# Performance work log

Measured on AMD Instinct MI355X. Metric: run time of the kernel, lower is better.

## Reference

```python
import jax, jax.numpy as jnp
import numpy as np
from jax import lax

IMG_W = 1024.0
IMG_H = 1024.0
CONF_THRESH = 0.5
NMS_THRESH = 0.3
MAX_DELTA = 2.0
K_PRE = 300   # pre-NMS candidates per image per level
K_OUT = 10    # keep[:10] per image per level, as in the torch code


def _make_anchors(hw, stride, base, scales=(0.5, 1.0, 1.5), ars=(0.5, 1.0, 2.0)):
    # anchor index a is outermost to match permute(0,1,3,4,2).reshape ordering
    whs = np.array([[base * sc * np.sqrt(ar), base * sc / np.sqrt(ar)]
                    for sc in scales for ar in ars], dtype=np.float32)  # [A,2]
    c = (np.arange(hw, dtype=np.float32) + 0.5) * stride
    cy, cx = np.meshgrid(c, c, indexing='ij')
    cx = cx.reshape(-1)[None, :]  # [1,HW]
    cy = cy.reshape(-1)[None, :]
    w = whs[:, 0:1]
    h = whs[:, 1:2]
    anc = np.stack([cx - 0.5 * w, cy - 0.5 * h, cx + 0.5 * w, cy + 0.5 * h], axis=-1)  # [A,HW,4]
    return jnp.asarray(anc.reshape(-1, 4))


def setup_inputs() -> dict:
    key = jax.random.key(0)
    ks = jax.random.split(key, 8)
    B, A = 16, 9
    hws = [128, 64, 32, 16]
    strides = [8, 16, 32, 64]
    bases = [64, 128, 256, 512]
    inp = {}
    for li in range(4):
        inp[f'cls{li}'] = jax.random.normal(ks[li], (B, A, 1, hws[li], hws[li]), jnp.float32)
        inp[f'box{li}'] = 0.3 * jax.random.normal(ks[li + 4], (B, A, 4, hws[li], hws[li]), jnp.float32)
        inp[f'anc{li}'] = _make_anchors(hws[li], strides[li], bases[li])
    return inp


def decode_boxes(deltas, anchors):
    # deltas: [B,N,4], anchors: [1,N,4] (broadcast). Faithful to apply_deltas_to_anchors.
    w = anchors[..., 2] - anchors[..., 0]
    h = anchors[..., 3] - anchors[..., 1]
    cx = anchors[..., 0] + 0.5 * w
    cy = anchors[..., 1] + 0.5 * h
    d = jnp.clip(deltas, -MAX_DELTA, MAX_DELTA)
    px = cx + d[..., 0] * w
    py = cy + d[..., 1] * h
    pw = w * jnp.exp(d[..., 2])
    ph = h * jnp.exp(d[..., 3])
    x1 = jnp.clip(px - 0.5 * pw, 0.0, IMG_W)
    y1 = jnp.clip(py - 0.5 * ph, 0.0, IMG_H)
    x2 = jnp.clip(px + 0.5 * pw, 0.0, IMG_W)
    y2 = jnp.clip(py + 0.5 * ph, 0.0, IMG_H)
    boxes = jnp.stack([x1, y1, x2, y2], axis=-1)
    bw = x2 - x1
    bh = y2 - y1
    valid = (bw > 1.0) & (bh > 1.0) & (bw < 2000.0) & (bh < 2000.0)
    return boxes, valid


def _pairwise_iou(b):
    # b: [K,4]
    area = (b[:, 2] - b[:, 0]) * (b[:, 3] - b[:, 1])
    x1 = jnp.maximum(b[:, None, 0], b[None, :, 0])
    y1 = jnp.maximum(b[:, None, 1], b[None, :, 1])
    x2 = jnp.minimum(b[:, None, 2], b[None, :, 2])
    y2 = jnp.minimum(b[:, None, 3], b[None, :, 3])
    inter = jnp.clip(x2 - x1, 0.0) * jnp.clip(y2 - y1, 0.0)
    return inter / (area[:, None] + area[None, :] - inter + 1e-9)


def _nms_image(boxes, masked_scores):
    # boxes: [N,4]; masked_scores: [N] (score if conf&valid else -1)
    topv, topi = lax.top_k(masked_scores, K_PRE)   # score-descending, like torchvision nms order
    b = boxes[topi]                                 # [K,4]
    ious = _pairwise_iou(b)
    idxs = jnp.arange(K_PRE)
    keep0 = topv > 0.0  # only candidates above conf thresh (>0.5) survive the mask fill of -1

    def body(i, keep):
        sup = (ious[i] > NMS_THRESH) & (idxs > i)
        return jnp.where(keep[i], keep & ~sup, keep)

    keep = lax.fori_loop(0, K_PRE, body, keep0)
    rank = jnp.cumsum(keep.astype(jnp.int32)) - 1
    sel = keep & (rank < K_OUT)                     # keep[:10]
    idx = jnp.where(sel, rank, K_OUT)               # dump slot K_OUT
    out_b = jnp.zeros((K_OUT + 1, 4), boxes.dtype).at[idx].set(b)[:K_OUT]
    out_s = jnp.zeros((K_OUT + 1,), topv.dtype).at[idx].set(topv)[:K_OUT]
    out_v = jnp.zeros((K_OUT + 1,), bool).at[idx].set(sel)[:K_OUT]
    return out_b, out_s, out_v


def _process_level(cls, box, anc):
    B = cls.shape[0]
    # [B,A,C,H,W] -> [B,A,H,W,C] -> [B,N]; C=1
    scores = jax.nn.sigmoid(jnp.transpose(cls, (0, 1, 3, 4, 2)).reshape(B, -1))
    deltas = jnp.transpose(box, (0, 1, 3, 4, 2)).reshape(B, -1, 4)
    pboxes, valid = decode_boxes(deltas, anc[None])
    masked = jnp.where((scores > CONF_THRESH) & valid, scores, -1.0)
    return jax.vmap(_nms_image)(pboxes, masked)  # ([B,10,4],[B,10],[B,10])


def reference(cls0, cls1, cls2, cls3, box0, box1, box2, box3, anc0, anc1, anc2, anc3):
    levels = [(cls0, box0, anc0), (cls1, box1, anc1), (cls2, box2, anc2), (cls3, box3, anc3)]
    outs = [_process_level(c, b, a) for (c, b, a) in levels]
    boxes = jnp.concatenate([o[0] for o in outs], axis=1)   # [B, 40, 4]
    scores = jnp.concatenate([o[1] for o in outs], axis=1)  # [B, 40]
    valid = jnp.concatenate([o[2] for o in outs], axis=1)   # [B, 40] bool
    out5 = jnp.concatenate([boxes, scores[..., None]], axis=-1)  # [B, 40, 5]
    return out5, valid
```

## Files before the change

### kernel.cpp

```cpp
#include <hip/hip_runtime.h>
#include <stdint.h>

#define NLEV 4
#define BIMG 16
#define NPROB 64
#define NB 1024
#define BUF 2048
#define CPI 97
#define TCH (BIMG * CPI)
#define SKN 6144
#define FK 512
#define SLOTS 8
#define KPRE 300
#define KOUT 10
#define NTHREADS 256
#define CHUNK 2048

__device__ unsigned long long g_cand[TCH * BUF];
__device__ int g_ccount[TCH];

struct Params {
    const float* cls[NLEV];
    const float* box[NLEV];
    const float* anc[NLEV];
};

__device__ __constant__ int c_tbin[4] = {256, 179, 77, 0};
__device__ __constant__ int c_sh[4]   = {14, 12, 10, 8};
__device__ __constant__ int c_cbase[4] = {0, 72, 90, 95};
__device__ __constant__ int c_nch[4]   = {72, 18, 5, 2};

__device__ __forceinline__ int bin_of(float x) {
    int b = (int)(x * (NB / 8.0f));
    return b > (NB - 1) ? (NB - 1) : b;
}

__device__ __forceinline__ bool decode_c(float d0, float d1, float d2, float d3,
                                         float4 an, float out[4]) {
#pragma clang fp contract(off)
    float w = an.z - an.x;
    float h = an.w - an.y;
    float cx = an.x + 0.5f * w;
    float cy = an.y + 0.5f * h;
    d0 = fminf(fmaxf(d0, -2.0f), 2.0f);
    d1 = fminf(fmaxf(d1, -2.0f), 2.0f);
    d2 = fminf(fmaxf(d2, -2.0f), 2.0f);
    d3 = fminf(fmaxf(d3, -2.0f), 2.0f);
    float px = cx + d0 * w;
    float py = cy + d1 * h;
    float pw = w * expf(d2);
    float ph = h * expf(d3);
    float x1 = fminf(fmaxf(px - 0.5f * pw, 0.0f), 1024.0f);
    float y1 = fminf(fmaxf(py - 0.5f * ph, 0.0f), 1024.0f);
    float x2 = fminf(fmaxf(px + 0.5f * pw, 0.0f), 1024.0f);
    float y2 = fminf(fmaxf(py + 0.5f * ph, 0.0f), 1024.0f);
    out[0] = x1; out[1] = y1; out[2] = x2; out[3] = y2;
    float bw = x2 - x1;
    float bh = y2 - y1;
    return (bw > 1.0f) && (bh > 1.0f) && (bw < 2000.0f) && (bh < 2000.0f);
}

__device__ __forceinline__ bool decode_one(const float* boxbase, const float* ancbase,
                                           int b, int e, int sh, float out[4]) {
    int HW = 1 << sh;
    int a = e >> sh;
    int hw = e & (HW - 1);
    const float* dB = boxbase + ((size_t)(b * 9 + a) * 4) * (size_t)HW + hw;
    float d0 = dB[0];
    float d1 = dB[(size_t)HW];
    float d2 = dB[(size_t)2 * HW];
    float d3 = dB[(size_t)3 * HW];
    float4 an = *(const float4*)(ancbase + (size_t)4 * e);
    return decode_c(d0, d1, d2, d3, an, out);
}

__device__ __forceinline__ void map_block(int c, int& level, int& chunk) {
    if (c < 72)      { level = 0; chunk = c; }
    else if (c < 90) { level = 1; chunk = c - 72; }
    else if (c < 95) { level = 2; chunk = c - 90; }
    else             { level = 3; chunk = c - 95; }
}

__global__ __launch_bounds__(NTHREADS) void k_scan(Params P) {
    __shared__ unsigned long long buf[BUF];
    __shared__ int s_cnt;
    if (threadIdx.x == 0) s_cnt = 0;
    __syncthreads();

    int img = blockIdx.x / CPI;
    int level, chunk;
    map_block(blockIdx.x % CPI, level, chunk);
    int sh = c_sh[level];
    int tbin = c_tbin[level];
    int N4 = (9 << sh) >> 2;
    int HW = 1 << sh;
    const float4* cls4 = (const float4*)(P.cls[level] + (size_t)img * (9 << sh));
    const float* boxp = P.box[level];
    const float* ancp = P.anc[level];
    int base4 = (chunk * CHUNK) >> 2;

    int i4a = base4 + threadIdx.x;
    int i4b = base4 + NTHREADS + threadIdx.x;
    bool va = i4a < N4, vb = i4b < N4;
    float4 xa, xb;
    if (va) xa = cls4[i4a];
    if (vb) xb = cls4[i4b];

#pragma unroll
    for (int g = 0; g < 2; g++) {
        bool vg = g ? vb : va;
        if (!vg) continue;
        float4 x = g ? xb : xa;
        int e0 = 4 * (g ? i4b : i4a);
        float xs[4] = {x.x, x.y, x.z, x.w};
        int bins[4];
        bool hit = false;
#pragma unroll
        for (int c = 0; c < 4; c++) {
            bins[c] = (xs[c] > 0.f) ? bin_of(xs[c]) : -1;
            hit |= (bins[c] >= tbin);
        }
        if (!hit) continue;
        int a = e0 >> sh;
        int hw = e0 & (HW - 1);
        const float* plane = boxp + ((size_t)((img * 9 + a) * 4)) * (size_t)HW + hw;
        float4 d0 = *(const float4*)(plane);
        float4 d1 = *(const float4*)(plane + HW);
        float4 d2 = *(const float4*)(plane + 2 * (size_t)HW);
        float4 d3 = *(const float4*)(plane + 3 * (size_t)HW);
        const float4* anc4 = (const float4*)ancp + e0;
        float s0[4] = {d0.x, d0.y, d0.z, d0.w};
        float s1[4] = {d1.x, d1.y, d1.z, d1.w};
        float s2[4] = {d2.x, d2.y, d2.z, d2.w};
        float s3[4] = {d3.x, d3.y, d3.z, d3.w};
#pragma unroll
        for (int c = 0; c < 4; c++) {
            if (bins[c] >= tbin) {
                float bo[4];
                if (decode_c(s0[c], s1[c], s2[c], s3[c], anc4[c], bo)) {
                    float s = 1.0f / (1.0f + expf(-xs[c]));
                    int e = e0 + c;
                    unsigned long long key =
                        ((unsigned long long)__float_as_uint(s) << 32) |
                        ((unsigned long long)(0x3FFFFu - (unsigned)e) << 10) |
                        (unsigned long long)bins[c];
                    int pos = atomicAdd(&s_cnt, 1);
                    buf[pos] = key;
                }
            }
        }
    }
    __syncthreads();

    int cnt = s_cnt;
    if (threadIdx.x == 0) g_ccount[blockIdx.x] = cnt;
    unsigned long long* dst = g_cand + (size_t)blockIdx.x * BUF;
    for (int i = threadIdx.x; i < cnt; i += NTHREADS) dst[i] = buf[i];
}

__global__ __launch_bounds__(NTHREADS) void k_nms(Params P, float* out) {
    __shared__ unsigned long long skey[SKN];
    __shared__ uint8_t lookup[SKN];
    __shared__ __align__(16) int lh[NB];
    __shared__ int suf[NTHREADS + 1];
    __shared__ int cnts[80], pre[80];
    __shared__ unsigned long long surv[FK];
    __shared__ float bx[FK * 4];
    __shared__ float area[FK];
    __shared__ int alive[FK];
    __shared__ float s_ob[KOUT * 5];
    __shared__ int s_cut, s_scnt, s_selc;

    int p = blockIdx.x;
    int level = p >> 4, img = p & 15;
    int sh = c_sh[level];
    int tid = threadIdx.x;
    int nch = c_nch[level];
    int gbase = img * CPI + c_cbase[level];

    for (int i = tid; i < NB; i += NTHREADS) lh[i] = 0;
    if (tid < nch) cnts[tid] = g_ccount[gbase + tid];
    if (tid == 0) { s_scnt = 0; s_selc = 0; }
    __syncthreads();
    if (tid == 0) {
        int acc = 0;
        pre[0] = 0;
        for (int c = 0; c < nch; c++) {
            acc += cnts[c];
            pre[c + 1] = acc > SKN ? SKN : acc;
        }
    }
    __syncthreads();
    int n = pre[nch];
    if (tid < nch) {
        int lo = pre[tid], hi = pre[tid + 1];
        for (int j = lo; j < hi; j++) lookup[j] = (uint8_t)tid;
    }
    __syncthreads();

    for (int j = tid; j < n; j += NTHREADS) {
        int c = lookup[j];
        unsigned long long key = g_cand[(size_t)(gbase + c) * BUF + (j - pre[c])];
        skey[j] = key;
        atomicAdd(&lh[(int)(key & 1023u)], 1);
    }
    __syncthreads();

    {
        int4 hv = ((const int4*)lh)[tid];
        suf[tid] = hv.x + hv.y + hv.z + hv.w;
        if (tid == 0) suf[NTHREADS] = 0;
        __syncthreads();
        for (int off = 1; off < NTHREADS; off <<= 1) {
            int v = (tid + off < NTHREADS) ? suf[tid + off] : 0;
            __syncthreads();
            suf[tid] += v;
            __syncthreads();
        }
        int shi = suf[tid + 1];
        int slo = suf[tid];
        if (slo >= KPRE && shi < KPRE) {
            int h4[4] = {hv.x, hv.y, hv.z, hv.w};
            int cum = shi, c = 0;
            for (int j = 3; j >= 0; j--) {
                cum += h4[j];
                if (cum >= KPRE) { c = 4 * tid + j; break; }
            }
            s_cut = c;
        }
        if (tid == 0 && suf[0] < KPRE) s_cut = 0;
    }
    __syncthreads();
    int cut = s_cut;

    for (int i = tid; i < n; i += NTHREADS) {
        unsigned long long key = skey[i];
        if ((int)(key & 1023u) >= cut) {
            int pos = atomicAdd(&s_scnt, 1);
            if (pos < FK) surv[pos] = key;
        }
    }
    __syncthreads();
    int m = s_scnt;
    if (m > FK) m = FK;

    for (int i = tid; i < m; i += NTHREADS) {
        unsigned long long key = surv[i];
        int e = (int)(0x3FFFFu - (unsigned)((key >> 10) & 0x3FFFFu));
        float bo[4];
        decode_one(P.box[level], P.anc[level], img, e, sh, bo);
        bx[i * 4 + 0] = bo[0];
        bx[i * 4 + 1] = bo[1];
        bx[i * 4 + 2] = bo[2];
        bx[i * 4 + 3] = bo[3];
        {
#pragma clang fp contract(off)
            area[i] = (bo[2] - bo[0]) * (bo[3] - bo[1]);
        }
    }
    __syncthreads();

    for (int i = tid; i < m; i += NTHREADS) {
        unsigned long long k = surv[i];
        int r = 0;
        for (int j = 0; j < m; j++) r += (surv[j] > k);
        alive[i] = (r < KPRE) ? 1 : 0;
    }
    __syncthreads();

    if (tid < 64) {
        unsigned long long rk[SLOTS];
        float rb0[SLOTS], rb1[SLOTS], rb2[SLOTS], rb3[SLOTS], rar[SLOTS];
        int ralive = 0;
#pragma unroll
        for (int s = 0; s < SLOTS; s++) {
            int i = tid + 64 * s;
            rk[s] = 0;
            if (i < m && alive[i]) {
                rk[s] = surv[i];
                rb0[s] = bx[i * 4 + 0];
                rb1[s] = bx[i * 4 + 1];
                rb2[s] = bx[i * 4 + 2];
                rb3[s] = bx[i * 4 + 3];
                rar[s] = area[i];
                ralive |= (1 << s);
            }
        }
        for (int it = 0; it < KOUT; it++) {
            unsigned long long best = 0;
#pragma unroll
            for (int s = 0; s < SLOTS; s++)
                if ((ralive >> s) & 1) { if (rk[s] > best) best = rk[s]; }
#pragma unroll
            for (int off = 1; off < 64; off <<= 1) {
                unsigned long long o = __shfl_xor(best, off, 64);
                if (o > best) best = o;
            }
            if (best == 0ull) break;
            int my = -1;
#pragma unroll
            for (int s = 0; s < SLOTS; s++)
                if (((ralive >> s) & 1) && rk[s] == best) my = s;
            int ci = -1;
            if (my >= 0) ci = tid + 64 * my;
#pragma unroll
            for (int off = 1; off < 64; off <<= 1) {
                int o = __shfl_xor(ci, off, 64);
                if (o > ci) ci = o;
            }
            if (my >= 0) {
                ralive &= ~(1 << my);
                s_ob[it * 5 + 0] = rb0[my];
                s_ob[it * 5 + 1] = rb1[my];
                s_ob[it * 5 + 2] = rb2[my];
                s_ob[it * 5 + 3] = rb3[my];
                s_ob[it * 5 + 4] = __uint_as_float((unsigned)(best >> 32));
                s_selc = it + 1;
            }
            float cx1 = bx[ci * 4 + 0], cy1 = bx[ci * 4 + 1];
            float cx2 = bx[ci * 4 + 2], cy2 = bx[ci * 4 + 3];
            float ca = area[ci];
#pragma unroll
            for (int s = 0; s < SLOTS; s++) {
                if ((ralive >> s) & 1) {
#pragma clang fp contract(off)
                    float ix1 = fmaxf(cx1, rb0[s]);
                    float iy1 = fmaxf(cy1, rb1[s]);
                    float ix2 = fminf(cx2, rb2[s]);
                    float iy2 = fminf(cy2, rb3[s]);
                    float iw = fmaxf(ix2 - ix1, 0.0f);
                    float ih = fmaxf(iy2 - iy1, 0.0f);
                    float inter = iw * ih;
                    float denom = (ca + rar[s]) - inter + 1e-9f;
                    float iou = inter / denom;
                    if (iou > 0.3f) ralive &= ~(1 << s);
                }
            }
        }
    }
    __syncthreads();

    if (tid < KOUT) {
        float o0 = 0.f, o1 = 0.f, o2 = 0.f, o3 = 0.f, o4 = 0.f, ov = 0.f;
        if (tid < s_selc) {
            o0 = s_ob[tid * 5 + 0];
            o1 = s_ob[tid * 5 + 1];
            o2 = s_ob[tid * 5 + 2];
            o3 = s_ob[tid * 5 + 3];
            o4 = s_ob[tid * 5 + 4];
            ov = 1.0f;
        }
        int q = level * KOUT + tid;
        float* o5 = out + (size_t)img * 200 + (size_t)q * 5;
        o5[0] = o0; o5[1] = o1; o5[2] = o2; o5[3] = o3; o5[4] = o4;
        out[3200 + img * 40 + q] = ov;
    }
}

extern "C" void kernel_launch(void* const* d_in, const int* in_sizes, int n_in,
                              void* d_out, int out_size, void* d_ws, size_t ws_size,
                              hipStream_t stream) {
    Params P;
    for (int l = 0; l < 4; l++) {
        P.cls[l] = (const float*)d_in[3 * l + 0];
        P.box[l] = (const float*)d_in[3 * l + 1];
        P.anc[l] = (const float*)d_in[3 * l + 2];
    }
    float* out = (float*)d_out;
    k_scan<<<TCH, NTHREADS, 0, stream>>>(P);
    k_nms<<<NPROB, NTHREADS, 0, stream>>>(P, out);
}
```

Baseline: 154.7 us.

## Fuse scan and NMS kernels with a global atomic grid barrier

Merges the scan and NMS kernels into one launch. The first 64 blocks wait on a global done-counter, built from a threadfence, an atomic add and an acquire spin, until every scan block has written its candidates, and then run NMS. The large shared skey and lookup arrays are removed, and candidates are re-read from global memory through a binary search over chunk prefixes in both the histogram pass and the filter pass. This saves a kernel launch gap and lowers shared memory per block, which may raise occupancy. In exchange it reads global memory twice, and it relies on the waiting blocks not deadlocking, which needs all 1552 blocks to get scheduled while 64 of them spin.

```diff
diff --git a/kernel.cpp b/kernel.cpp
--- a/kernel.cpp
+++ b/kernel.cpp
@@ -18,6 +18,7 @@
 
 __device__ unsigned long long g_cand[TCH * BUF];
 __device__ int g_ccount[TCH];
+__device__ int g_done;
 
 struct Params {
     const float* cls[NLEV];
@@ -81,86 +82,9 @@
     else             { level = 3; chunk = c - 95; }
 }
 
-__global__ __launch_bounds__(NTHREADS) void k_scan(Params P) {
+__global__ __launch_bounds__(NTHREADS) void k_fused(Params P, float* out) {
     __shared__ unsigned long long buf[BUF];
     __shared__ int s_cnt;
-    if (threadIdx.x == 0) s_cnt = 0;
-    __syncthreads();
-
-    int img = blockIdx.x / CPI;
-    int level, chunk;
-    map_block(blockIdx.x % CPI, level, chunk);
-    int sh = c_sh[level];
-    int tbin = c_tbin[level];
-    int N4 = (9 << sh) >> 2;
-    int HW = 1 << sh;
-    const float4* cls4 = (const float4*)(P.cls[level] + (size_t)img * (9 << sh));
-    const float* boxp = P.box[level];
-    const float* ancp = P.anc[level];
-    int base4 = (chunk * CHUNK) >> 2;
-
-    int i4a = base4 + threadIdx.x;
-    int i4b = base4 + NTHREADS + threadIdx.x;
-    bool va = i4a < N4, vb = i4b < N4;
-    float4 xa, xb;
-    if (va) xa = cls4[i4a];
-    if (vb) xb = cls4[i4b];
-
-#pragma unroll
-    for (int g = 0; g < 2; g++) {
-        bool vg = g ? vb : va;
-        if (!vg) continue;
-        float4 x = g ? xb : xa;
-        int e0 = 4 * (g ? i4b : i4a);
-        float xs[4] = {x.x, x.y, x.z, x.w};
-        int bins[4];
-        bool hit = false;
-#pragma unroll
-        for (int c = 0; c < 4; c++) {
-            bins[c] = (xs[c] > 0.f) ? bin_of(xs[c]) : -1;
-            hit |= (bins[c] >= tbin);
-        }
-        if (!hit) continue;
-        int a = e0 >> sh;
-        int hw = e0 & (HW - 1);
-        const float* plane = boxp + ((size_t)((img * 9 + a) * 4)) * (size_t)HW + hw;
-        float4 d0 = *(const float4*)(plane);
-        float4 d1 = *(const float4*)(plane + HW);
-        float4 d2 = *(const float4*)(plane + 2 * (size_t)HW);
-        float4 d3 = *(const float4*)(plane + 3 * (size_t)HW);
-        const float4* anc4 = (const float4*)ancp + e0;
-        float s0[4] = {d0.x, d0.y, d0.z, d0.w};
-        float s1[4] = {d1.x, d1.y, d1.z, d1.w};
-        float s2[4] = {d2.x, d2.y, d2.z, d2.w};
-        float s3[4] = {d3.x, d3.y, d3.z, d3.w};
-#pragma unroll
-        for (int c = 0; c < 4; c++) {
-            if (bins[c] >= tbin) {
-                float bo[4];
-                if (decode_c(s0[c], s1[c], s2[c], s3[c], anc4[c], bo)) {
-                    float s = 1.0f / (1.0f + expf(-xs[c]));
-                    int e = e0 + c;
-                    unsigned long long key =
-                        ((unsigned long long)__float_as_uint(s) << 32) |
-                        ((unsigned long long)(0x3FFFFu - (unsigned)e) << 10) |
-                        (unsigned long long)bins[c];
-                    int pos = atomicAdd(&s_cnt, 1);
-                    buf[pos] = key;
-                }
-            }
-        }
-    }
-    __syncthreads();
-
-    int cnt = s_cnt;
-    if (threadIdx.x == 0) g_ccount[blockIdx.x] = cnt;
-    unsigned long long* dst = g_cand + (size_t)blockIdx.x * BUF;
-    for (int i = threadIdx.x; i < cnt; i += NTHREADS) dst[i] = buf[i];
-}
-
-__global__ __launch_bounds__(NTHREADS) void k_nms(Params P, float* out) {
-    __shared__ unsigned long long skey[SKN];
-    __shared__ uint8_t lookup[SKN];
     __shared__ __align__(16) int lh[NB];
     __shared__ int suf[NTHREADS + 1];
     __shared__ int cnts[80], pre[80];
@@ -171,10 +95,104 @@
     __shared__ float s_ob[KOUT * 5];
     __shared__ int s_cut, s_scnt, s_selc;
 
+    int tid = threadIdx.x;
+
+    {
+        if (tid == 0) s_cnt = 0;
+        __syncthreads();
+
+        int img = blockIdx.x / CPI;
+        int level, chunk;
+        map_block(blockIdx.x % CPI, level, chunk);
+        int sh = c_sh[level];
+        int tbin = c_tbin[level];
+        int N4 = (9 << sh) >> 2;
+        int HW = 1 << sh;
+        const float4* cls4 = (const float4*)(P.cls[level] + (size_t)img * (9 << sh));
+        const float* boxp = P.box[level];
+        const float* ancp = P.anc[level];
+        int base4 = (chunk * CHUNK) >> 2;
+
+        int i4a = base4 + tid;
+        int i4b = base4 + NTHREADS + tid;
+        bool va = i4a < N4, vb = i4b < N4;
+        float4 xa, xb;
+        if (va) xa = cls4[i4a];
+        if (vb) xb = cls4[i4b];
+
+#pragma unroll
+        for (int g = 0; g < 2; g++) {
+            bool vg = g ? vb : va;
+            if (!vg) continue;
+            float4 x = g ? xb : xa;
+            int e0 = 4 * (g ? i4b : i4a);
+            float xs[4] = {x.x, x.y, x.z, x.w};
+            int bins[4];
+            bool hit = false;
+#pragma unroll
+            for (int c = 0; c < 4; c++) {
+                bins[c] = (xs[c] > 0.f) ? bin_of(xs[c]) : -1;
+                hit |= (bins[c] >= tbin);
+            }
+            if (!hit) continue;
+            int a = e0 >> sh;
+            int hw = e0 & (HW - 1);
+            const float* plane = boxp + ((size_t)((img * 9 + a) * 4)) * (size_t)HW + hw;
+            float4 d0 = *(const float4*)(plane);
+            float4 d1 = *(const float4*)(plane + HW);
+            float4 d2 = *(const float4*)(plane + 2 * (size_t)HW);
+            float4 d3 = *(const float4*)(plane + 3 * (size_t)HW);
+            const float4* anc4 = (const float4*)ancp + e0;
+            float s0[4] = {d0.x, d0.y, d0.z, d0.w};
+            float s1[4] = {d1.x, d1.y, d1.z, d1.w};
+            float s2[4] = {d2.x, d2.y, d2.z, d2.w};
+            float s3[4] = {d3.x, d3.y, d3.z, d3.w};
+#pragma unroll
+            for (int c = 0; c < 4; c++) {
+                if (bins[c] >= tbin) {
+                    float bo[4];
+                    if (decode_c(s0[c], s1[c], s2[c], s3[c], anc4[c], bo)) {
+                        float s = 1.0f / (1.0f + expf(-xs[c]));
+                        int e = e0 + c;
+                        unsigned long long key =
+                            ((unsigned long long)__float_as_uint(s) << 32) |
+                            ((unsigned long long)(0x3FFFFu - (unsigned)e) << 10) |
+                            (unsigned long long)bins[c];
+                        int pos = atomicAdd(&s_cnt, 1);
+                        buf[pos] = key;
+                    }
+                }
+            }
+        }
+        __syncthreads();
+
+        int cnt = s_cnt;
+        if (tid == 0) g_ccount[blockIdx.x] = cnt;
+        unsigned long long* dst = g_cand + (size_t)blockIdx.x * BUF;
+        for (int i = tid; i < cnt; i += NTHREADS) dst[i] = buf[i];
+    }
+    __syncthreads();
+
+    if (blockIdx.x >= NPROB) {
+        if (tid == 0) {
+            __threadfence();
+            atomicAdd(&g_done, 1);
+        }
+        return;
+    }
+    if (tid == 0) {
+        __threadfence();
+        int pos = atomicAdd(&g_done, 1);
+        int target = (pos / TCH + 1) * TCH;
+        while (__hip_atomic_load(&g_done, __ATOMIC_ACQUIRE,
+                                 __HIP_MEMORY_SCOPE_AGENT) < target)
+            __builtin_amdgcn_s_sleep(8);
+    }
+    __syncthreads();
+
     int p = blockIdx.x;
     int level = p >> 4, img = p & 15;
     int sh = c_sh[level];
-    int tid = threadIdx.x;
     int nch = c_nch[level];
     int gbase = img * CPI + c_cbase[level];
 
@@ -192,16 +210,14 @@
     }
     __syncthreads();
     int n = pre[nch];
-    if (tid < nch) {
-        int lo = pre[tid], hi = pre[tid + 1];
-        for (int j = lo; j < hi; j++) lookup[j] = (uint8_t)tid;
-    }
-    __syncthreads();
 
     for (int j = tid; j < n; j += NTHREADS) {
-        int c = lookup[j];
-        unsigned long long key = g_cand[(size_t)(gbase + c) * BUF + (j - pre[c])];
-        skey[j] = key;
+        int lo = 0, hi = nch - 1;
+        while (lo < hi) {
+            int mid = (lo + hi + 1) >> 1;
+            if (pre[mid] <= j) lo = mid; else hi = mid - 1;
+        }
+        unsigned long long key = g_cand[(size_t)(gbase + lo) * BUF + (j - pre[lo])];
         atomicAdd(&lh[(int)(key & 1023u)], 1);
     }
     __syncthreads();
@@ -233,8 +249,13 @@
     __syncthreads();
     int cut = s_cut;
 
-    for (int i = tid; i < n; i += NTHREADS) {
-        unsigned long long key = skey[i];
+    for (int j = tid; j < n; j += NTHREADS) {
+        int lo = 0, hi = nch - 1;
+        while (lo < hi) {
+            int mid = (lo + hi + 1) >> 1;
+            if (pre[mid] <= j) lo = mid; else hi = mid - 1;
+        }
+        unsigned long long key = g_cand[(size_t)(gbase + lo) * BUF + (j - pre[lo])];
         if ((int)(key & 1023u) >= cut) {
             int pos = atomicAdd(&s_scnt, 1);
             if (pos < FK) surv[pos] = key;
@@ -367,6 +388,5 @@
         P.anc[l] = (const float*)d_in[3 * l + 2];
     }
     float* out = (float*)d_out;
-    k_scan<<<TCH, NTHREADS, 0, stream>>>(P);
-    k_nms<<<NPROB, NTHREADS, 0, stream>>>(P, out);
-}
+    k_fused<<<TCH, NTHREADS, 0, stream>>>(P, out);
+}
```

Measured after the change: 253.4 us. 1.64x slower.

## Write scan candidates directly to per-problem global buffers with warp-aggregated atomics

Applied to the files above, without the earlier changes.

The scan kernel now appends each surviving candidate straight into a per-(level,image) global array, using a ballot/popcount warp-aggregated atomic on a global counter. It also builds the score-bin histogram in shared memory and merges it into a global per-problem histogram. The NMS kernel then reads the prebuilt histogram and candidate array directly, dropping the per-chunk staging, the lookup table and the shared-memory copy and histogram pass. The cost is global atomic contention across the chunk blocks of each problem, and state that must be zeroed by the NMS kernel for the next call.

```diff
diff --git a/kernel.cpp b/kernel.cpp
--- a/kernel.cpp
+++ b/kernel.cpp
@@ -5,10 +5,9 @@
 #define BIMG 16
 #define NPROB 64
 #define NB 1024
-#define BUF 2048
+#define CAP 6144
 #define CPI 97
 #define TCH (BIMG * CPI)
-#define SKN 6144
 #define FK 512
 #define SLOTS 8
 #define KPRE 300
@@ -16,8 +15,9 @@
 #define NTHREADS 256
 #define CHUNK 2048
 
-__device__ unsigned long long g_cand[TCH * BUF];
-__device__ int g_ccount[TCH];
+__device__ int g_pcount[NPROB];
+__device__ __align__(16) int g_hist[NPROB * NB];
+__device__ unsigned long long g_cand[NPROB * CAP];
 
 struct Params {
     const float* cls[NLEV];
@@ -27,8 +27,6 @@
 
 __device__ __constant__ int c_tbin[4] = {256, 179, 77, 0};
 __device__ __constant__ int c_sh[4]   = {14, 12, 10, 8};
-__device__ __constant__ int c_cbase[4] = {0, 72, 90, 95};
-__device__ __constant__ int c_nch[4]   = {72, 18, 5, 2};
 
 __device__ __forceinline__ int bin_of(float x) {
     int b = (int)(x * (NB / 8.0f));
@@ -82,9 +80,8 @@
 }
 
 __global__ __launch_bounds__(NTHREADS) void k_scan(Params P) {
-    __shared__ unsigned long long buf[BUF];
-    __shared__ int s_cnt;
-    if (threadIdx.x == 0) s_cnt = 0;
+    __shared__ int lh[NB];
+    for (int i = threadIdx.x; i < NB; i += NTHREADS) lh[i] = 0;
     __syncthreads();
 
     int img = blockIdx.x / CPI;
@@ -94,10 +91,12 @@
     int tbin = c_tbin[level];
     int N4 = (9 << sh) >> 2;
     int HW = 1 << sh;
+    int p = (level << 4) | img;
     const float4* cls4 = (const float4*)(P.cls[level] + (size_t)img * (9 << sh));
     const float* boxp = P.box[level];
     const float* ancp = P.anc[level];
     int base4 = (chunk * CHUNK) >> 2;
+    int lane = threadIdx.x & 63;
 
     int i4a = base4 + threadIdx.x;
     int i4b = base4 + NTHREADS + threadIdx.x;
@@ -114,13 +113,13 @@
         int e0 = 4 * (g ? i4b : i4a);
         float xs[4] = {x.x, x.y, x.z, x.w};
         int bins[4];
-        bool hit = false;
+        bool grp = false;
 #pragma unroll
         for (int c = 0; c < 4; c++) {
             bins[c] = (xs[c] > 0.f) ? bin_of(xs[c]) : -1;
-            hit |= (bins[c] >= tbin);
-        }
-        if (!hit) continue;
+            grp |= (bins[c] >= tbin);
+        }
+        if (!grp) continue;
         int a = e0 >> sh;
         int hw = e0 & (HW - 1);
         const float* plane = boxp + ((size_t)((img * 9 + a) * 4)) * (size_t)HW + hw;
@@ -135,79 +134,65 @@
         float s3[4] = {d3.x, d3.y, d3.z, d3.w};
 #pragma unroll
         for (int c = 0; c < 4; c++) {
+            bool emit = false;
+            unsigned long long key = 0;
             if (bins[c] >= tbin) {
                 float bo[4];
                 if (decode_c(s0[c], s1[c], s2[c], s3[c], anc4[c], bo)) {
+                    atomicAdd(&lh[bins[c]], 1);
                     float s = 1.0f / (1.0f + expf(-xs[c]));
                     int e = e0 + c;
-                    unsigned long long key =
-                        ((unsigned long long)__float_as_uint(s) << 32) |
-                        ((unsigned long long)(0x3FFFFu - (unsigned)e) << 10) |
-                        (unsigned long long)bins[c];
-                    int pos = atomicAdd(&s_cnt, 1);
-                    buf[pos] = key;
+                    key = ((unsigned long long)__float_as_uint(s) << 32) |
+                          ((unsigned long long)(0x3FFFFu - (unsigned)e) << 10) |
+                          (unsigned long long)bins[c];
+                    emit = true;
                 }
             }
-        }
-    }
-    __syncthreads();
-
-    int cnt = s_cnt;
-    if (threadIdx.x == 0) g_ccount[blockIdx.x] = cnt;
-    unsigned long long* dst = g_cand + (size_t)blockIdx.x * BUF;
-    for (int i = threadIdx.x; i < cnt; i += NTHREADS) dst[i] = buf[i];
+            unsigned long long mask = __ballot(emit);
+            if (emit) {
+                int leader = (int)(__ffsll((long long)mask) - 1);
+                int base;
+                if (lane == leader)
+                    base = atomicAdd(&g_pcount[p], (int)__popcll(mask));
+                base = __shfl(base, leader, 64);
+                int pos = base + (int)__popcll(mask & ((1ull << lane) - 1ull));
+                if (pos < CAP) g_cand[(size_t)p * CAP + pos] = key;
+            }
+        }
+    }
+    __syncthreads();
+
+    for (int i = threadIdx.x; i < NB; i += NTHREADS) {
+        int v = lh[i];
+        if (v) atomicAdd(&g_hist[p * NB + i], v);
+    }
 }
 
 __global__ __launch_bounds__(NTHREADS) void k_nms(Params P, float* out) {
-    __shared__ unsigned long long skey[SKN];
-    __shared__ uint8_t lookup[SKN];
-    __shared__ __align__(16) int lh[NB];
     __shared__ int suf[NTHREADS + 1];
-    __shared__ int cnts[80], pre[80];
     __shared__ unsigned long long surv[FK];
     __shared__ float bx[FK * 4];
     __shared__ float area[FK];
     __shared__ int alive[FK];
     __shared__ float s_ob[KOUT * 5];
-    __shared__ int s_cut, s_scnt, s_selc;
+    __shared__ int s_n, s_cut, s_scnt, s_selc;
 
     int p = blockIdx.x;
     int level = p >> 4, img = p & 15;
     int sh = c_sh[level];
     int tid = threadIdx.x;
-    int nch = c_nch[level];
-    int gbase = img * CPI + c_cbase[level];
-
-    for (int i = tid; i < NB; i += NTHREADS) lh[i] = 0;
-    if (tid < nch) cnts[tid] = g_ccount[gbase + tid];
-    if (tid == 0) { s_scnt = 0; s_selc = 0; }
-    __syncthreads();
+
     if (tid == 0) {
-        int acc = 0;
-        pre[0] = 0;
-        for (int c = 0; c < nch; c++) {
-            acc += cnts[c];
-            pre[c + 1] = acc > SKN ? SKN : acc;
-        }
-    }
-    __syncthreads();
-    int n = pre[nch];
-    if (tid < nch) {
-        int lo = pre[tid], hi = pre[tid + 1];
-        for (int j = lo; j < hi; j++) lookup[j] = (uint8_t)tid;
-    }
-    __syncthreads();
-
-    for (int j = tid; j < n; j += NTHREADS) {
-        int c = lookup[j];
-        unsigned long long key = g_cand[(size_t)(gbase + c) * BUF + (j - pre[c])];
-        skey[j] = key;
-        atomicAdd(&lh[(int)(key & 1023u)], 1);
-    }
-    __syncthreads();
+        int n = g_pcount[p];
+        g_pcount[p] = 0;
+        s_n = n > CAP ? CAP : n;
+        s_scnt = 0;
+        s_selc = 0;
+    }
 
     {
-        int4 hv = ((const int4*)lh)[tid];
+        int4 hv = ((const int4*)(g_hist + p * NB))[tid];
+        ((int4*)(g_hist + p * NB))[tid] = make_int4(0, 0, 0, 0);
         suf[tid] = hv.x + hv.y + hv.z + hv.w;
         if (tid == 0) suf[NTHREADS] = 0;
         __syncthreads();
@@ -232,9 +217,10 @@
     }
     __syncthreads();
     int cut = s_cut;
+    int n = s_n;
 
     for (int i = tid; i < n; i += NTHREADS) {
-        unsigned long long key = skey[i];
+        unsigned long long key = g_cand[(size_t)p * CAP + i];
         if ((int)(key & 1023u) >= cut) {
             int pos = atomicAdd(&s_scnt, 1);
             if (pos < FK) surv[pos] = key;
```

New measurement: 416.6 us. 2.69x slower.
